# Performance work log

Hardware: AMD Instinct MI355X
Metric: run time of the kernel (lower is better)

The kernel has to match this reference:

```python
import jax, jax.numpy as jnp
import numpy as np

TEMPERATURE = 0.05
BETA = 1.0
LAMBDA_THRESHOLD = 0.7


def setup_inputs() -> dict:
    key = jax.random.key(0)
    k1, k2 = jax.random.split(key)
    B, D = 8192, 256
    features = jax.random.normal(k1, (B, D), dtype=jnp.float32)
    labels = jax.random.randint(k2, (B,), 0, 100, dtype=jnp.int64)
    return {"features": features, "labels": labels}


def reference(features, labels):
    B = features.shape[0]
    eps = 1e-12
    # L2 normalize rows
    f = features / jnp.maximum(jnp.linalg.norm(features, axis=1, keepdims=True), eps)
    sim = jnp.matmul(f, f.T) / TEMPERATURE                      # [B, B]
    sim_max = jnp.max(sim, axis=1, keepdims=True)               # [B, 1]
    sim_stable = sim - sim_max

    same = (labels[:, None] == labels[None, :])
    eye = jnp.eye(B, dtype=bool)
    pos_mask = same & ~eye                                       # [B, B] bool

    # Denominator: logsumexp over all non-self entries per row
    exp_sim = jnp.exp(sim_stable) * (~eye)
    log_denom = jnp.log(jnp.sum(exp_sim, axis=1, keepdims=True) + eps) + sim_max  # [B,1]

    # SCL term: mean over positive pairs of (log_denom[i] - sim[i,j])
    pos_f = pos_mask.astype(sim.dtype)
    n_pos = jnp.sum(pos_f)
    scl_sum = jnp.sum(pos_f * (log_denom - sim))
    scl_loss = jnp.where(n_pos > 0, scl_sum / jnp.maximum(n_pos, 1.0), 0.0)

    # Relaxation term: per row, logsumexp over high-sim positive logits + baseline
    high = (sim * TEMPERATURE > LAMBDA_THRESHOLD) & pos_mask     # [B, B] bool
    neg_inf = jnp.asarray(-jnp.inf, sim.dtype)
    masked_logits = jnp.where(high, sim_stable, neg_inf)          # [B, B]
    baseline = (1.0 / TEMPERATURE) - sim_max                      # [B, 1]
    all_logits = jnp.concatenate([masked_logits, baseline], axis=1)  # [B, B+1]
    row_lse = jax.nn.logsumexp(all_logits, axis=1)                # [B]
    row_has = jnp.any(high, axis=1)
    n_high = jnp.sum(high.astype(sim.dtype))
    relax_sum = jnp.sum(jnp.where(row_has, row_lse, 0.0))
    relaxation_loss = jnp.where(n_high > 0, relax_sum / jnp.maximum(n_high, 1.0), 0.0)

    total = scl_loss + BETA * relaxation_loss
    return jnp.clip(total, 0.0, 10.0)
```

## Files before the change

kernel.cpp:

```cpp
#include <hip/hip_runtime.h>
#include <hip/hip_bf16.h>
#include <math.h>

#define B_N 8192
#define D_K 256
#define TILE 128
#define NT 512
#define NBLK 64
#define NPAIR 2080
#define NCLS 100
#define KEXP 28.8539008177792681f

typedef __attribute__((ext_vector_type(8))) short short8;
typedef __attribute__((ext_vector_type(4))) float f32x4;

__device__ __forceinline__ unsigned short f2bf(float x) {
    unsigned int u = __float_as_uint(x);
    unsigned int r = (u + 0x7FFFu + ((u >> 16) & 1u)) >> 16;
    return (unsigned short)r;
}

__device__ __forceinline__ void gload_lds16(const short* g, short* l) {
    __builtin_amdgcn_global_load_lds(
        (const __attribute__((address_space(1))) void*)g,
        (__attribute__((address_space(3))) void*)l, 16, 0, 0);
}

__device__ __forceinline__ float row_sum16(float v) {
    v += __int_as_float(__builtin_amdgcn_update_dpp(0, __float_as_int(v), 0xB1, 0xF, 0xF, true));
    v += __int_as_float(__builtin_amdgcn_update_dpp(0, __float_as_int(v), 0x4E, 0xF, 0xF, true));
    v += __int_as_float(__builtin_amdgcn_update_dpp(0, __float_as_int(v), 0x141, 0xF, 0xF, true));
    v += __int_as_float(__builtin_amdgcn_update_dpp(0, __float_as_int(v), 0x140, 0xF, 0xF, true));
    return v;
}

__global__ void prep_kernel(const float* __restrict__ feat, unsigned short* __restrict__ fnorm,
                            const int* __restrict__ labels, int* __restrict__ cnt,
                            float* __restrict__ gscal, double* __restrict__ accum,
                            unsigned int* __restrict__ done) {
    if (blockIdx.x == 0) {
        __shared__ int h[NCLS];
        int t = threadIdx.x;
        if (t < NCLS) h[t] = 0;
        if (t == 0) {
            gscal[0] = 0.f; gscal[1] = 0.f;
            accum[0] = 0.0; accum[1] = 0.0; accum[2] = 0.0;
            *done = 0u;
        }
        __syncthreads();
        for (int r = t; r < B_N; r += 256) atomicAdd(&h[labels[r]], 1);
        __syncthreads();
        if (t < NCLS) cnt[t] = h[t];
    }
    int wave = threadIdx.x >> 6, lane = threadIdx.x & 63;
    int row = blockIdx.x * 4 + wave;
    float4 v = *(const float4*)(feat + (size_t)row * D_K + lane * 4);
    float ss = v.x * v.x + v.y * v.y + v.z * v.z + v.w * v.w;
    #pragma unroll
    for (int off = 1; off < 64; off <<= 1) ss += __shfl_xor(ss, off);
    float inv = 1.0f / fmaxf(sqrtf(ss), 1e-12f);
    ushort4 o;
    o.x = f2bf(v.x * inv); o.y = f2bf(v.y * inv);
    o.z = f2bf(v.z * inv); o.w = f2bf(v.w * inv);
    *(ushort4*)(fnorm + (size_t)row * D_K + lane * 4) = o;
}

__global__ __launch_bounds__(NT, 4) void main_kernel(
        const unsigned short* __restrict__ fnorm, const int* __restrict__ labels,
        float2* __restrict__ G, float* __restrict__ gscal) {
    int bid = blockIdx.x;
    int b = (int)((sqrtf(8.0f * bid + 1.0f) - 1.0f) * 0.5f);
    while ((b + 1) * (b + 2) / 2 <= bid) ++b;
    while (b * (b + 1) / 2 > bid) --b;
    int a = bid - b * (b + 1) / 2;
    const int row0 = a * TILE, col0 = b * TILE;
    const bool diag = (a == b);

    __shared__ short As[TILE * 64];
    __shared__ short Bs[TILE * 64];
    __shared__ int Ls[2 * TILE];
    __shared__ int ghs[8];
    __shared__ float gps[8];

    const int tid = threadIdx.x;
    const int lane = tid & 63, wave = tid >> 6;
    const int wm = wave >> 2, wn = wave & 3;
    const int l15 = lane & 15, lhi = lane >> 4;
    const short* fn = (const short*)fnorm;

    if (tid < 128) Ls[tid] = labels[row0 + tid];
    else if (tid < 256) Ls[tid] = labels[col0 + tid - 128];
    if (lane == 0) ghs[wave] = 0;

    f32x4 acc[4][2];
    #pragma unroll
    for (int i = 0; i < 4; i++)
        #pragma unroll
        for (int j = 0; j < 2; j++) acc[i][j] = {0.f, 0.f, 0.f, 0.f};

    for (int kc = 0; kc < 4; ++kc) {
        #pragma unroll
        for (int li = 0; li < 2; ++li) {
            int id = tid + li * NT;
            int r = id >> 3, c = id & 7;
            int cs = c ^ (r & 7);
            int ub = (id & ~63) * 8;
            gload_lds16(fn + (size_t)(row0 + r) * D_K + kc * 64 + cs * 8, &As[ub]);
            if (!diag)
                gload_lds16(fn + (size_t)(col0 + r) * D_K + kc * 64 + cs * 8, &Bs[ub]);
        }
        __syncthreads();
        const short* Bsrc = diag ? As : Bs;
        #pragma unroll
        for (int ks = 0; ks < 2; ++ks) {
            short8 af[4], bfr[2];
            #pragma unroll
            for (int mi = 0; mi < 4; mi++) {
                int row = wm * 64 + mi * 16 + l15;
                int ch = (ks * 4 + lhi) ^ (l15 & 7);
                af[mi] = *(const short8*)&As[row * 64 + ch * 8];
            }
            #pragma unroll
            for (int ni = 0; ni < 2; ni++) {
                int row = wn * 32 + ni * 16 + l15;
                int ch = (ks * 4 + lhi) ^ (l15 & 7);
                bfr[ni] = *(const short8*)&Bsrc[row * 64 + ch * 8];
            }
            #pragma unroll
            for (int mi = 0; mi < 4; mi++)
                #pragma unroll
                for (int ni = 0; ni < 2; ni++)
                    acc[mi][ni] = __builtin_amdgcn_mfma_f32_16x16x32_bf16(af[mi], bfr[ni], acc[mi][ni], 0, 0, 0);
        }
        __syncthreads();
    }

    float2* Rbuf = (float2*)As;
    float2* Cbuf = (float2*)Bs;

    int lc[2], colg[2];
    #pragma unroll
    for (int ni = 0; ni < 2; ni++) {
        int c = wn * 32 + ni * 16 + l15;
        lc[ni] = Ls[128 + c];
        colg[ni] = col0 + c;
    }

    float cD[2] = {0.f, 0.f};
    float gp = 0.f;
    unsigned int hmask = 0;

    #pragma unroll
    for (int mi = 0; mi < 4; mi++) {
        #pragma unroll
        for (int reg = 0; reg < 4; reg++) {
            int rloc = wm * 64 + mi * 16 + lhi * 4 + reg;
            int rowg = row0 + rloc;
            int lr = Ls[rloc];
            float d = 0.f;
            #pragma unroll
            for (int ni = 0; ni < 2; ni++) {
                float dot = acc[mi][ni][reg];
                float e = __builtin_exp2f((dot - 1.0f) * KEXP);
                bool ns = (rowg != colg[ni]);
                float ev = ns ? e : 0.f;
                d += ev; cD[ni] += ev;
                bool ps = ns && (lr == lc[ni]);
                gp += ps ? dot : 0.f;
                bool hi = ps && (dot > 0.7f);
                hmask |= hi ? (1u << ((mi * 4 + reg) * 2 + ni)) : 0u;
            }
            d = row_sum16(d);
            if (l15 == 0) Rbuf[wn * 128 + rloc] = {d, 0.f};
        }
    }

    if (!diag) {
        #pragma unroll
        for (int ni = 0; ni < 2; ni++) {
            cD[ni] += __shfl_xor(cD[ni], 16);
            cD[ni] += __shfl_xor(cD[ni], 32);
        }
        if (lhi == 0) {
            #pragma unroll
            for (int ni = 0; ni < 2; ni++)
                Cbuf[wm * 128 + wn * 32 + ni * 16 + l15] = {cD[ni], 0.f};
        }
    }

    gp = row_sum16(gp);
    gp += __shfl_xor(gp, 16);
    gp += __shfl_xor(gp, 32);
    if (lane == 0) gps[wave] = gp;

    if (__any(hmask != 0)) {
        float cR[2] = {0.f, 0.f};
        #pragma unroll
        for (int mi = 0; mi < 4; mi++) {
            #pragma unroll
            for (int reg = 0; reg < 4; reg++) {
                int rloc = wm * 64 + mi * 16 + lhi * 4 + reg;
                float rx = 0.f;
                #pragma unroll
                for (int ni = 0; ni < 2; ni++) {
                    if (hmask & (1u << ((mi * 4 + reg) * 2 + ni))) {
                        float e = __builtin_exp2f((acc[mi][ni][reg] - 1.0f) * KEXP);
                        rx += e; cR[ni] += e;
                    }
                }
                rx = row_sum16(rx);
                if (l15 == 0) Rbuf[wn * 128 + rloc].y = rx;
            }
        }
        if (!diag) {
            #pragma unroll
            for (int ni = 0; ni < 2; ni++) {
                cR[ni] += __shfl_xor(cR[ni], 16);
                cR[ni] += __shfl_xor(cR[ni], 32);
            }
            if (lhi == 0) {
                #pragma unroll
                for (int ni = 0; ni < 2; ni++)
                    Cbuf[wm * 128 + wn * 32 + ni * 16 + l15].y = cR[ni];
            }
        }
        int nhi = __popc(hmask);
        #pragma unroll
        for (int off = 1; off < 64; off <<= 1) nhi += __shfl_xor(nhi, off);
        if (lane == 0) ghs[wave] = nhi;
    }
    __syncthreads();

    if (tid < 128) {
        int r = tid;
        float2 a0 = Rbuf[r], a1 = Rbuf[128 + r], a2 = Rbuf[256 + r], a3 = Rbuf[384 + r];
        G[(size_t)b * B_N + row0 + r] = {a0.x + a1.x + a2.x + a3.x, a0.y + a1.y + a2.y + a3.y};
    } else if (tid < 256 && !diag) {
        int c = tid - 128;
        float2 a0 = Cbuf[c], a1 = Cbuf[128 + c];
        G[(size_t)a * B_N + col0 + c] = {a0.x + a1.x, a0.y + a1.y};
    }
    if (tid == 0) {
        float w = diag ? 1.0f : 2.0f;
        float gpt = gps[0] + gps[1] + gps[2] + gps[3] + gps[4] + gps[5] + gps[6] + gps[7];
        atomicAdd(&gscal[0], w * gpt);
        int tot = ghs[0] + ghs[1] + ghs[2] + ghs[3] + ghs[4] + ghs[5] + ghs[6] + ghs[7];
        if (tot > 0) atomicAdd(&gscal[1], w * (float)tot);
    }
}

__global__ void finalize_kernel(const float2* __restrict__ G, const int* __restrict__ labels,
                                const int* __restrict__ cnt, const float* __restrict__ gscal,
                                double* __restrict__ accum, unsigned int* __restrict__ done,
                                float* __restrict__ out) {
    int lane = threadIdx.x & 63, q = threadIdx.x >> 6;
    int r = blockIdx.x * 64 + lane;
    float d = 0.f, rx = 0.f;
    #pragma unroll
    for (int s = 0; s < 16; ++s) {
        float2 g = G[(size_t)(q * 16 + s) * B_N + r];
        d += g.x; rx += g.y;
    }
    __shared__ float2 sh[4][64];
    sh[q][lane] = {d, rx};
    __syncthreads();
    if (threadIdx.x < 64) {
        int rr = blockIdx.x * 64 + threadIdx.x;
        float2 t0 = sh[0][threadIdx.x], t1 = sh[1][threadIdx.x];
        float2 t2 = sh[2][threadIdx.x], t3 = sh[3][threadIdx.x];
        float dd = t0.x + t1.x + t2.x + t3.x;
        float rr2 = t0.y + t1.y + t2.y + t3.y;
        float np = (float)(cnt[labels[rr]] - 1);
        float ld = logf(dd + 1e-12f) + 20.0f;
        double s1 = (double)np * (double)ld;
        double s2 = (double)np;
        double s3 = (rr2 > 0.f) ? (double)logf(rr2 + 1.0f) : 0.0;
        #pragma unroll
        for (int off = 1; off < 64; off <<= 1) {
            s1 += __shfl_xor(s1, off);
            s2 += __shfl_xor(s2, off);
            s3 += __shfl_xor(s3, off);
        }
        if (threadIdx.x == 0) {
            atomicAdd(&accum[0], s1);
            atomicAdd(&accum[1], s2);
            atomicAdd(&accum[2], s3);
            __threadfence();
            unsigned int tk = atomicAdd(done, 1u);
            if (tk == gridDim.x - 1) {
                double a1 = atomicAdd(&accum[0], 0.0);
                double a2 = atomicAdd(&accum[1], 0.0);
                double a3 = atomicAdd(&accum[2], 0.0);
                double gp = (double)gscal[0];
                double gh = (double)gscal[1];
                double scl = (a2 > 0.0) ? (a1 - 20.0 * gp) / fmax(a2, 1.0) : 0.0;
                double rel = (gh > 0.0) ? a3 / fmax(gh, 1.0) : 0.0;
                double tot = scl + rel;
                tot = fmin(fmax(tot, 0.0), 10.0);
                out[0] = (float)tot;
            }
        }
    }
}

extern "C" void kernel_launch(void* const* d_in, const int* in_sizes, int n_in,
                              void* d_out, int out_size, void* d_ws, size_t ws_size,
                              hipStream_t stream) {
    const float* feat = (const float*)d_in[0];
    const int* labels = (const int*)d_in[1];
    float* out = (float*)d_out;
    char* ws = (char*)d_ws;

    unsigned short* fnorm = (unsigned short*)(ws);
    float2* G          = (float2*)(ws + (size_t)4 * 1024 * 1024);
    int*    cnt        = (int*)(ws + (size_t)8 * 1024 * 1024);
    float*  gscal      = (float*)(ws + (size_t)8 * 1024 * 1024 + 1024);
    double* accum      = (double*)(ws + (size_t)8 * 1024 * 1024 + 2048);
    unsigned int* done = (unsigned int*)(ws + (size_t)8 * 1024 * 1024 + 3072);

    prep_kernel<<<B_N / 4, 256, 0, stream>>>(feat, fnorm, labels, cnt, gscal, accum, done);
    main_kernel<<<NPAIR, NT, 0, stream>>>(fnorm, labels, G, gscal);
    finalize_kernel<<<B_N / 64, 256, 0, stream>>>(G, labels, cnt, gscal, accum, done, out);
    (void)in_sizes; (void)n_in; (void)out_size; (void)ws_size;
}
```

Baseline: 124.1 us.

## Double-buffer LDS tiles to prefetch next K chunk during MFMA compute

Splits the A and B shared-memory tiles into two buffers. The first K chunk is loaded before the loop, and each iteration issues async global-to-LDS loads for the next chunk before running the MFMAs on the current one. This drops one barrier per iteration and is meant to hide global load latency behind matrix math. The cost is twice the LDS per block, which can lower how many blocks fit per CU, and the K loop has only four chunks.

```diff
diff --git a/kernel.cpp b/kernel.cpp
--- a/kernel.cpp
+++ b/kernel.cpp
@@ -76,8 +76,8 @@
     const int row0 = a * TILE, col0 = b * TILE;
     const bool diag = (a == b);
 
-    __shared__ short As[TILE * 64];
-    __shared__ short Bs[TILE * 64];
+    __shared__ short As[2][TILE * 64];
+    __shared__ short Bs[2][TILE * 64];
     __shared__ int Ls[2 * TILE];
     __shared__ int ghs[8];
     __shared__ float gps[8];
@@ -88,29 +88,44 @@
     const int l15 = lane & 15, lhi = lane >> 4;
     const short* fn = (const short*)fnorm;
 
+    const int id0 = tid, id1 = tid + NT;
+    const int r0s = id0 >> 3, c0s = (id0 & 7) ^ (r0s & 7), u0 = (id0 & ~63) * 8;
+    const int r1s = id1 >> 3, c1s = (id1 & 7) ^ (r1s & 7), u1 = (id1 & ~63) * 8;
+
     if (tid < 128) Ls[tid] = labels[row0 + tid];
     else if (tid < 256) Ls[tid] = labels[col0 + tid - 128];
     if (lane == 0) ghs[wave] = 0;
 
+    {
+        gload_lds16(fn + (size_t)(row0 + r0s) * D_K + c0s * 8, &As[0][u0]);
+        gload_lds16(fn + (size_t)(row0 + r1s) * D_K + c1s * 8, &As[0][u1]);
+        if (!diag) {
+            gload_lds16(fn + (size_t)(col0 + r0s) * D_K + c0s * 8, &Bs[0][u0]);
+            gload_lds16(fn + (size_t)(col0 + r1s) * D_K + c1s * 8, &Bs[0][u1]);
+        }
+    }
+
     f32x4 acc[4][2];
     #pragma unroll
     for (int i = 0; i < 4; i++)
         #pragma unroll
         for (int j = 0; j < 2; j++) acc[i][j] = {0.f, 0.f, 0.f, 0.f};
 
+    #pragma unroll
     for (int kc = 0; kc < 4; ++kc) {
-        #pragma unroll
-        for (int li = 0; li < 2; ++li) {
-            int id = tid + li * NT;
-            int r = id >> 3, c = id & 7;
-            int cs = c ^ (r & 7);
-            int ub = (id & ~63) * 8;
-            gload_lds16(fn + (size_t)(row0 + r) * D_K + kc * 64 + cs * 8, &As[ub]);
-            if (!diag)
-                gload_lds16(fn + (size_t)(col0 + r) * D_K + kc * 64 + cs * 8, &Bs[ub]);
-        }
+        const int cur = kc & 1;
         __syncthreads();
-        const short* Bsrc = diag ? As : Bs;
+        if (kc < 3) {
+            const int nxt = cur ^ 1, ko = (kc + 1) * 64;
+            gload_lds16(fn + (size_t)(row0 + r0s) * D_K + ko + c0s * 8, &As[nxt][u0]);
+            gload_lds16(fn + (size_t)(row0 + r1s) * D_K + ko + c1s * 8, &As[nxt][u1]);
+            if (!diag) {
+                gload_lds16(fn + (size_t)(col0 + r0s) * D_K + ko + c0s * 8, &Bs[nxt][u0]);
+                gload_lds16(fn + (size_t)(col0 + r1s) * D_K + ko + c1s * 8, &Bs[nxt][u1]);
+            }
+        }
+        const short* Asrc = As[cur];
+        const short* Bsrc = diag ? As[cur] : Bs[cur];
         #pragma unroll
         for (int ks = 0; ks < 2; ++ks) {
             short8 af[4], bfr[2];
@@ -118,7 +133,7 @@
             for (int mi = 0; mi < 4; mi++) {
                 int row = wm * 64 + mi * 16 + l15;
                 int ch = (ks * 4 + lhi) ^ (l15 & 7);
-                af[mi] = *(const short8*)&As[row * 64 + ch * 8];
+                af[mi] = *(const short8*)&Asrc[row * 64 + ch * 8];
             }
             #pragma unroll
             for (int ni = 0; ni < 2; ni++) {
@@ -132,11 +147,11 @@
                 for (int ni = 0; ni < 2; ni++)
                     acc[mi][ni] = __builtin_amdgcn_mfma_f32_16x16x32_bf16(af[mi], bfr[ni], acc[mi][ni], 0, 0, 0);
         }
-        __syncthreads();
-    }
-
-    float2* Rbuf = (float2*)As;
-    float2* Cbuf = (float2*)Bs;
+    }
+    __syncthreads();
+
+    float2* Rbuf = (float2*)As[0];
+    float2* Cbuf = (float2*)Bs[0];
 
     int lc[2], colg[2];
     #pragma unroll
```

New measurement: 122.1 us. Within noise of the previous version (-1.6%).

## Switch main tile to 32x32x16 MFMA with 16 waves per block

Applied to the files above, without the earlier changes.

Doubles the block to 1024 threads (16 waves in a 4x4 grid), each computing one 32x32 sub-tile with the 32x32x16 bf16 MFMA instead of a 64x32 sub-tile built from 16x16x32 MFMAs. Each thread now issues a single LDS load per operand tile and holds 16 accumulator floats instead of 32. The epilogue is rewritten for the new accumulator layout, with an extra cross-lane shuffle per row sum and four column partials to combine. This aims at lower register pressure and higher occupancy, at the cost of more waves sharing the same LDS tile and less register-level operand reuse per wave.

```diff
diff --git a/kernel.cpp b/kernel.cpp
--- a/kernel.cpp
+++ b/kernel.cpp
@@ -5,14 +5,14 @@
 #define B_N 8192
 #define D_K 256
 #define TILE 128
-#define NT 512
+#define NT 1024
 #define NBLK 64
 #define NPAIR 2080
 #define NCLS 100
 #define KEXP 28.8539008177792681f
 
 typedef __attribute__((ext_vector_type(8))) short short8;
-typedef __attribute__((ext_vector_type(4))) float f32x4;
+typedef __attribute__((ext_vector_type(16))) float f32x16;
 
 __device__ __forceinline__ unsigned short f2bf(float x) {
     unsigned int u = __float_as_uint(x);
@@ -65,7 +65,7 @@
     *(ushort4*)(fnorm + (size_t)row * D_K + lane * 4) = o;
 }
 
-__global__ __launch_bounds__(NT, 4) void main_kernel(
+__global__ __launch_bounds__(NT, 8) void main_kernel(
         const unsigned short* __restrict__ fnorm, const int* __restrict__ labels,
         float2* __restrict__ G, float* __restrict__ gscal) {
     int bid = blockIdx.x;
@@ -79,58 +79,39 @@
     __shared__ short As[TILE * 64];
     __shared__ short Bs[TILE * 64];
     __shared__ int Ls[2 * TILE];
-    __shared__ int ghs[8];
-    __shared__ float gps[8];
+    __shared__ int ghs[16];
+    __shared__ float gps[16];
 
     const int tid = threadIdx.x;
     const int lane = tid & 63, wave = tid >> 6;
     const int wm = wave >> 2, wn = wave & 3;
-    const int l15 = lane & 15, lhi = lane >> 4;
+    const int l31 = lane & 31, lhf = lane >> 5;
     const short* fn = (const short*)fnorm;
+
+    const int rs = tid >> 3, cs = (tid & 7) ^ (rs & 7);
+    const int ub = (tid & ~63) * 8;
 
     if (tid < 128) Ls[tid] = labels[row0 + tid];
     else if (tid < 256) Ls[tid] = labels[col0 + tid - 128];
     if (lane == 0) ghs[wave] = 0;
 
-    f32x4 acc[4][2];
-    #pragma unroll
-    for (int i = 0; i < 4; i++)
-        #pragma unroll
-        for (int j = 0; j < 2; j++) acc[i][j] = {0.f, 0.f, 0.f, 0.f};
+    f32x16 acc;
+    #pragma unroll
+    for (int i = 0; i < 16; i++) acc[i] = 0.f;
 
     for (int kc = 0; kc < 4; ++kc) {
-        #pragma unroll
-        for (int li = 0; li < 2; ++li) {
-            int id = tid + li * NT;
-            int r = id >> 3, c = id & 7;
-            int cs = c ^ (r & 7);
-            int ub = (id & ~63) * 8;
-            gload_lds16(fn + (size_t)(row0 + r) * D_K + kc * 64 + cs * 8, &As[ub]);
-            if (!diag)
-                gload_lds16(fn + (size_t)(col0 + r) * D_K + kc * 64 + cs * 8, &Bs[ub]);
-        }
+        gload_lds16(fn + (size_t)(row0 + rs) * D_K + kc * 64 + cs * 8, &As[ub]);
+        if (!diag)
+            gload_lds16(fn + (size_t)(col0 + rs) * D_K + kc * 64 + cs * 8, &Bs[ub]);
         __syncthreads();
         const short* Bsrc = diag ? As : Bs;
-        #pragma unroll
-        for (int ks = 0; ks < 2; ++ks) {
-            short8 af[4], bfr[2];
-            #pragma unroll
-            for (int mi = 0; mi < 4; mi++) {
-                int row = wm * 64 + mi * 16 + l15;
-                int ch = (ks * 4 + lhi) ^ (l15 & 7);
-                af[mi] = *(const short8*)&As[row * 64 + ch * 8];
-            }
-            #pragma unroll
-            for (int ni = 0; ni < 2; ni++) {
-                int row = wn * 32 + ni * 16 + l15;
-                int ch = (ks * 4 + lhi) ^ (l15 & 7);
-                bfr[ni] = *(const short8*)&Bsrc[row * 64 + ch * 8];
-            }
-            #pragma unroll
-            for (int mi = 0; mi < 4; mi++)
-                #pragma unroll
-                for (int ni = 0; ni < 2; ni++)
-                    acc[mi][ni] = __builtin_amdgcn_mfma_f32_16x16x32_bf16(af[mi], bfr[ni], acc[mi][ni], 0, 0, 0);
+        const int arow = wm * 32 + l31, brow = wn * 32 + l31;
+        #pragma unroll
+        for (int kch = 0; kch < 4; ++kch) {
+            int cha = (kch * 2 + lhf) ^ (l31 & 7);
+            short8 af = *(const short8*)&As[arow * 64 + cha * 8];
+            short8 bf = *(const short8*)&Bsrc[brow * 64 + cha * 8];
+            acc = __builtin_amdgcn_mfma_f32_32x32x16_bf16(af, bf, acc, 0, 0, 0);
         }
         __syncthreads();
     }
@@ -138,54 +119,34 @@
     float2* Rbuf = (float2*)As;
     float2* Cbuf = (float2*)Bs;
 
-    int lc[2], colg[2];
-    #pragma unroll
-    for (int ni = 0; ni < 2; ni++) {
-        int c = wn * 32 + ni * 16 + l15;
-        lc[ni] = Ls[128 + c];
-        colg[ni] = col0 + c;
-    }
-
-    float cD[2] = {0.f, 0.f};
-    float gp = 0.f;
+    const int colg = col0 + wn * 32 + l31;
+    const int lc = Ls[128 + wn * 32 + l31];
+
+    float cD = 0.f, gp = 0.f;
     unsigned int hmask = 0;
 
     #pragma unroll
-    for (int mi = 0; mi < 4; mi++) {
-        #pragma unroll
-        for (int reg = 0; reg < 4; reg++) {
-            int rloc = wm * 64 + mi * 16 + lhi * 4 + reg;
-            int rowg = row0 + rloc;
-            int lr = Ls[rloc];
-            float d = 0.f;
-            #pragma unroll
-            for (int ni = 0; ni < 2; ni++) {
-                float dot = acc[mi][ni][reg];
-                float e = __builtin_exp2f((dot - 1.0f) * KEXP);
-                bool ns = (rowg != colg[ni]);
-                float ev = ns ? e : 0.f;
-                d += ev; cD[ni] += ev;
-                bool ps = ns && (lr == lc[ni]);
-                gp += ps ? dot : 0.f;
-                bool hi = ps && (dot > 0.7f);
-                hmask |= hi ? (1u << ((mi * 4 + reg) * 2 + ni)) : 0u;
-            }
-            d = row_sum16(d);
-            if (l15 == 0) Rbuf[wn * 128 + rloc] = {d, 0.f};
-        }
+    for (int reg = 0; reg < 16; reg++) {
+        int rloc = wm * 32 + (reg & 3) + 8 * (reg >> 2) + 4 * lhf;
+        int rowg = row0 + rloc;
+        int lr = Ls[rloc];
+        float dot = acc[reg];
+        float e = __builtin_exp2f((dot - 1.0f) * KEXP);
+        bool ns = (rowg != colg);
+        float ev = ns ? e : 0.f;
+        cD += ev;
+        bool ps = ns && (lr == lc);
+        gp += ps ? dot : 0.f;
+        bool hi = ps && (dot > 0.7f);
+        hmask |= hi ? (1u << reg) : 0u;
+        float d = row_sum16(ev);
+        d += __shfl_xor(d, 16);
+        if (l31 == 0) Rbuf[wn * 128 + rloc] = {d, 0.f};
     }
 
     if (!diag) {
-        #pragma unroll
-        for (int ni = 0; ni < 2; ni++) {
-            cD[ni] += __shfl_xor(cD[ni], 16);
-            cD[ni] += __shfl_xor(cD[ni], 32);
-        }
-        if (lhi == 0) {
-            #pragma unroll
-            for (int ni = 0; ni < 2; ni++)
-                Cbuf[wm * 128 + wn * 32 + ni * 16 + l15] = {cD[ni], 0.f};
-        }
+        cD += __shfl_xor(cD, 32);
+        if (lhf == 0) Cbuf[wm * 128 + wn * 32 + l31] = {cD, 0.f};
     }
 
     gp = row_sum16(gp);
@@ -194,35 +155,22 @@
     if (lane == 0) gps[wave] = gp;
 
     if (__any(hmask != 0)) {
-        float cR[2] = {0.f, 0.f};
-        #pragma unroll
-        for (int mi = 0; mi < 4; mi++) {
-            #pragma unroll
-            for (int reg = 0; reg < 4; reg++) {
-                int rloc = wm * 64 + mi * 16 + lhi * 4 + reg;
-                float rx = 0.f;
-                #pragma unroll
-                for (int ni = 0; ni < 2; ni++) {
-                    if (hmask & (1u << ((mi * 4 + reg) * 2 + ni))) {
-                        float e = __builtin_exp2f((acc[mi][ni][reg] - 1.0f) * KEXP);
-                        rx += e; cR[ni] += e;
-                    }
-                }
-                rx = row_sum16(rx);
-                if (l15 == 0) Rbuf[wn * 128 + rloc].y = rx;
+        float cR = 0.f;
+        #pragma unroll
+        for (int reg = 0; reg < 16; reg++) {
+            int rloc = wm * 32 + (reg & 3) + 8 * (reg >> 2) + 4 * lhf;
+            float rx = 0.f;
+            if (hmask & (1u << reg)) {
+                rx = __builtin_exp2f((acc[reg] - 1.0f) * KEXP);
+                cR += rx;
             }
+            rx = row_sum16(rx);
+            rx += __shfl_xor(rx, 16);
+            if (l31 == 0) Rbuf[wn * 128 + rloc].y = rx;
         }
         if (!diag) {
-            #pragma unroll
-            for (int ni = 0; ni < 2; ni++) {
-                cR[ni] += __shfl_xor(cR[ni], 16);
-                cR[ni] += __shfl_xor(cR[ni], 32);
-            }
-            if (lhi == 0) {
-                #pragma unroll
-                for (int ni = 0; ni < 2; ni++)
-                    Cbuf[wm * 128 + wn * 32 + ni * 16 + l15].y = cR[ni];
-            }
+            cR += __shfl_xor(cR, 32);
+            if (lhf == 0) Cbuf[wm * 128 + wn * 32 + l31].y = cR;
         }
         int nhi = __popc(hmask);
         #pragma unroll
@@ -237,14 +185,16 @@
         G[(size_t)b * B_N + row0 + r] = {a0.x + a1.x + a2.x + a3.x, a0.y + a1.y + a2.y + a3.y};
     } else if (tid < 256 && !diag) {
         int c = tid - 128;
-        float2 a0 = Cbuf[c], a1 = Cbuf[128 + c];
-        G[(size_t)a * B_N + col0 + c] = {a0.x + a1.x, a0.y + a1.y};
+        float2 a0 = Cbuf[c], a1 = Cbuf[128 + c], a2 = Cbuf[256 + c], a3 = Cbuf[384 + c];
+        G[(size_t)a * B_N + col0 + c] = {a0.x + a1.x + a2.x + a3.x, a0.y + a1.y + a2.y + a3.y};
     }
     if (tid == 0) {
         float w = diag ? 1.0f : 2.0f;
-        float gpt = gps[0] + gps[1] + gps[2] + gps[3] + gps[4] + gps[5] + gps[6] + gps[7];
+        float gpt = 0.f;
+        int tot = 0;
+        #pragma unroll
+        for (int i = 0; i < 16; i++) { gpt += gps[i]; tot += ghs[i]; }
         atomicAdd(&gscal[0], w * gpt);
-        int tot = ghs[0] + ghs[1] + ghs[2] + ghs[3] + ghs[4] + ghs[5] + ghs[6] + ghs[7];
         if (tot > 0) atomicAdd(&gscal[1], w * (float)tot);
     }
 }
```

Result: slower. 136.9 us (+10.4%).

## Split each 128x128 tile pair into two 128x64 blocks of 256 threads

Applied to the files above, without the earlier changes.

Each triangular tile pair is now handled by two blocks, each covering half of the column range with 4 waves instead of 8. The grid doubles, per-block LDS shrinks, and the launch-bounds occupancy hint rises from 4 to 5 blocks. Partial sums are stored in twice as many G slots, so the finalize kernel reduces 32 slots per row instead of 16. The aim is better load balance and occupancy across CUs. The cost is loading the A tile twice per pair, plus extra partial-sum traffic and slightly more reduction work.

```diff
diff --git a/kernel.cpp b/kernel.cpp
--- a/kernel.cpp
+++ b/kernel.cpp
@@ -5,9 +5,10 @@
 #define B_N 8192
 #define D_K 256
 #define TILE 128
-#define NT 512
+#define NT 256
 #define NBLK 64
 #define NPAIR 2080
+#define NSLOT 128
 #define NCLS 100
 #define KEXP 28.8539008177792681f
 
@@ -65,31 +66,32 @@
     *(ushort4*)(fnorm + (size_t)row * D_K + lane * 4) = o;
 }
 
-__global__ __launch_bounds__(NT, 4) void main_kernel(
+__global__ __launch_bounds__(NT, 5) void main_kernel(
         const unsigned short* __restrict__ fnorm, const int* __restrict__ labels,
         float2* __restrict__ G, float* __restrict__ gscal) {
-    int bid = blockIdx.x;
-    int b = (int)((sqrtf(8.0f * bid + 1.0f) - 1.0f) * 0.5f);
-    while ((b + 1) * (b + 2) / 2 <= bid) ++b;
-    while (b * (b + 1) / 2 > bid) --b;
-    int a = bid - b * (b + 1) / 2;
-    const int row0 = a * TILE, col0 = b * TILE;
+    int pair = blockIdx.x >> 1, z = blockIdx.x & 1;
+    int b = (int)((sqrtf(8.0f * pair + 1.0f) - 1.0f) * 0.5f);
+    while ((b + 1) * (b + 2) / 2 <= pair) ++b;
+    while (b * (b + 1) / 2 > pair) --b;
+    int a = pair - b * (b + 1) / 2;
+    const int row0 = a * TILE;
+    const int col0 = b * TILE + z * 64;
     const bool diag = (a == b);
 
     __shared__ short As[TILE * 64];
-    __shared__ short Bs[TILE * 64];
-    __shared__ int Ls[2 * TILE];
-    __shared__ int ghs[8];
-    __shared__ float gps[8];
+    __shared__ short Bs[64 * 64];
+    __shared__ int Ls[TILE + 64];
+    __shared__ int ghs[4];
+    __shared__ float gps[4];
 
     const int tid = threadIdx.x;
     const int lane = tid & 63, wave = tid >> 6;
-    const int wm = wave >> 2, wn = wave & 3;
+    const int wm = wave >> 1, wn = wave & 1;
     const int l15 = lane & 15, lhi = lane >> 4;
     const short* fn = (const short*)fnorm;
 
     if (tid < 128) Ls[tid] = labels[row0 + tid];
-    else if (tid < 256) Ls[tid] = labels[col0 + tid - 128];
+    else if (tid < 192) Ls[tid] = labels[col0 + tid - 128];
     if (lane == 0) ghs[wave] = 0;
 
     f32x4 acc[4][2];
@@ -100,17 +102,23 @@
 
     for (int kc = 0; kc < 4; ++kc) {
         #pragma unroll
-        for (int li = 0; li < 2; ++li) {
+        for (int li = 0; li < 4; ++li) {
             int id = tid + li * NT;
-            int r = id >> 3, c = id & 7;
-            int cs = c ^ (r & 7);
+            int r = id >> 3, cs = (id & 7) ^ (r & 7);
             int ub = (id & ~63) * 8;
             gload_lds16(fn + (size_t)(row0 + r) * D_K + kc * 64 + cs * 8, &As[ub]);
-            if (!diag)
+        }
+        if (!diag) {
+            #pragma unroll
+            for (int li = 0; li < 2; ++li) {
+                int id = tid + li * NT;
+                int r = id >> 3, cs = (id & 7) ^ (r & 7);
+                int ub = (id & ~63) * 8;
                 gload_lds16(fn + (size_t)(col0 + r) * D_K + kc * 64 + cs * 8, &Bs[ub]);
+            }
         }
         __syncthreads();
-        const short* Bsrc = diag ? As : Bs;
+        const short* Bsrc = diag ? &As[z * 64 * 64] : Bs;
         #pragma unroll
         for (int ks = 0; ks < 2; ++ks) {
             short8 af[4], bfr[2];
@@ -184,7 +192,7 @@
         if (lhi == 0) {
             #pragma unroll
             for (int ni = 0; ni < 2; ni++)
-                Cbuf[wm * 128 + wn * 32 + ni * 16 + l15] = {cD[ni], 0.f};
+                Cbuf[wm * 64 + wn * 32 + ni * 16 + l15] = {cD[ni], 0.f};
         }
     }
 
@@ -221,7 +229,7 @@
             if (lhi == 0) {
                 #pragma unroll
                 for (int ni = 0; ni < 2; ni++)
-                    Cbuf[wm * 128 + wn * 32 + ni * 16 + l15].y = cR[ni];
+                    Cbuf[wm * 64 + wn * 32 + ni * 16 + l15].y = cR[ni];
             }
         }
         int nhi = __popc(hmask);
@@ -233,18 +241,17 @@
 
     if (tid < 128) {
         int r = tid;
-        float2 a0 = Rbuf[r], a1 = Rbuf[128 + r], a2 = Rbuf[256 + r], a3 = Rbuf[384 + r];
-        G[(size_t)b * B_N + row0 + r] = {a0.x + a1.x + a2.x + a3.x, a0.y + a1.y + a2.y + a3.y};
-    } else if (tid < 256 && !diag) {
-        int c = tid - 128;
-        float2 a0 = Cbuf[c], a1 = Cbuf[128 + c];
-        G[(size_t)a * B_N + col0 + c] = {a0.x + a1.x, a0.y + a1.y};
+        float2 a0 = Rbuf[r], a1 = Rbuf[128 + r];
+        G[(size_t)(b * 2 + z) * B_N + row0 + r] = {a0.x + a1.x, a0.y + a1.y};
+    } else if (!diag) {
+        int idx = tid - 128;
+        int wmi = idx >> 6, c = idx & 63;
+        G[(size_t)(a * 2 + wmi) * B_N + col0 + c] = Cbuf[wmi * 64 + c];
     }
     if (tid == 0) {
         float w = diag ? 1.0f : 2.0f;
-        float gpt = gps[0] + gps[1] + gps[2] + gps[3] + gps[4] + gps[5] + gps[6] + gps[7];
-        atomicAdd(&gscal[0], w * gpt);
-        int tot = ghs[0] + ghs[1] + ghs[2] + ghs[3] + ghs[4] + ghs[5] + ghs[6] + ghs[7];
+        atomicAdd(&gscal[0], w * (gps[0] + gps[1] + gps[2] + gps[3]));
+        int tot = ghs[0] + ghs[1] + ghs[2] + ghs[3];
         if (tot > 0) atomicAdd(&gscal[1], w * (float)tot);
     }
 }
@@ -257,8 +264,8 @@
     int r = blockIdx.x * 64 + lane;
     float d = 0.f, rx = 0.f;
     #pragma unroll
-    for (int s = 0; s < 16; ++s) {
-        float2 g = G[(size_t)(q * 16 + s) * B_N + r];
+    for (int s = 0; s < 32; ++s) {
+        float2 g = G[(size_t)(q * 32 + s) * B_N + r];
         d += g.x; rx += g.y;
     }
     __shared__ float2 sh[4][64];
@@ -313,13 +320,13 @@
 
     unsigned short* fnorm = (unsigned short*)(ws);
     float2* G          = (float2*)(ws + (size_t)4 * 1024 * 1024);
-    int*    cnt        = (int*)(ws + (size_t)8 * 1024 * 1024);
-    float*  gscal      = (float*)(ws + (size_t)8 * 1024 * 1024 + 1024);
-    double* accum      = (double*)(ws + (size_t)8 * 1024 * 1024 + 2048);
-    unsigned int* done = (unsigned int*)(ws + (size_t)8 * 1024 * 1024 + 3072);
+    int*    cnt        = (int*)(ws + (size_t)12 * 1024 * 1024);
+    float*  gscal      = (float*)(ws + (size_t)12 * 1024 * 1024 + 1024);
+    double* accum      = (double*)(ws + (size_t)12 * 1024 * 1024 + 2048);
+    unsigned int* done = (unsigned int*)(ws + (size_t)12 * 1024 * 1024 + 3072);
 
     prep_kernel<<<B_N / 4, 256, 0, stream>>>(feat, fnorm, labels, cnt, gscal, accum, done);
-    main_kernel<<<NPAIR, NT, 0, stream>>>(fnorm, labels, G, gscal);
+    main_kernel<<<NPAIR * 2, NT, 0, stream>>>(fnorm, labels, G, gscal);
     finalize_kernel<<<B_N / 64, 256, 0, stream>>>(G, labels, cnt, gscal, accum, done, out);
     (void)in_sizes; (void)n_in; (void)out_size; (void)ws_size;
 }
```

Result: slower. 147.7 us (+19.0%).
